# Kernel tuning notes

Measured on AMD Instinct MI355X. Metric: run time of the kernel, lower is better.

The kernel has to match this reference:

```python
import jax, jax.numpy as jnp
import numpy as np

B, C, H, W = 8, 64, 64, 64
R = 4
INTER = C // R   # 16
QK = C // 8      # 8
OUT = 64
EPS = 1e-5

def _bn(h, s, b, m, v):
    # inference-mode BatchNorm2d over channel dim of NCHW
    inv = s / jnp.sqrt(v + EPS)
    return h * inv[None, :, None, None] + (b - m * inv)[None, :, None, None]

def _conv1x1(h, w, b):
    # 1x1 conv == per-pixel matmul over channels
    return jnp.einsum('oc,bchw->bohw', w, h) + b[None, :, None, None]

def setup_inputs() -> dict:
    key = jax.random.key(0)
    ks = jax.random.split(key, 16)
    def wgt(k, shape):
        return jax.random.normal(k, shape, jnp.float32) * 0.05
    ones = lambda n: jnp.ones((n,), jnp.float32)
    zeros = lambda n: jnp.zeros((n,), jnp.float32)
    return {
        'x': jax.random.normal(ks[0], (B, C, H, W), jnp.float32),
        'lw1': wgt(ks[1], (INTER, C)), 'lb1': zeros(INTER),
        'ls1': ones(INTER), 'lbb1': zeros(INTER), 'lm1': zeros(INTER), 'lv1': ones(INTER),
        'lw2': wgt(ks[2], (C, INTER)), 'lb2': zeros(C),
        'ls2': ones(C), 'lbb2': zeros(C), 'lm2': zeros(C), 'lv2': ones(C),
        'gw1': wgt(ks[3], (INTER, C)), 'gb1': zeros(INTER),
        'gs1': ones(INTER), 'gbb1': zeros(INTER), 'gm1': zeros(INTER), 'gv1': ones(INTER),
        'gw2': wgt(ks[4], (C, INTER)), 'gb2': zeros(C),
        'gs2': ones(C), 'gbb2': zeros(C), 'gm2': zeros(C), 'gv2': ones(C),
        'qw': wgt(ks[5], (QK, C)), 'qb': zeros(QK),
        'kw': wgt(ks[6], (QK, C)), 'kb': zeros(QK),
        'vw': wgt(ks[7], (C, C)), 'vb': zeros(C),
        'gamma': jnp.zeros((1,), jnp.float32),  # torch init: zeros
        'cw': wgt(ks[8], (OUT, C, 3, 3)), 'cb': zeros(OUT),
        'cs': ones(OUT), 'cbb': zeros(OUT), 'cm': zeros(OUT), 'cv': ones(OUT),
    }

def reference(x, lw1, lb1, ls1, lbb1, lm1, lv1, lw2, lb2, ls2, lbb2, lm2, lv2,
              gw1, gb1, gs1, gbb1, gm1, gv1, gw2, gb2, gs2, gbb2, gm2, gv2,
              qw, qb, kw, kb, vw, vb, gamma, cw, cb, cs, cbb, cm, cv):
    # --- SE-style channel gating: local branch (per-pixel) + global branch (GAP) ---
    xl = _bn(_conv1x1(jax.nn.relu(_bn(_conv1x1(x, lw1, lb1), ls1, lbb1, lm1, lv1)), lw2, lb2),
             ls2, lbb2, lm2, lv2)
    g = x.mean(axis=(2, 3), keepdims=True)  # AdaptiveAvgPool2d(1) -> [B,C,1,1]
    xg = _bn(_conv1x1(jax.nn.relu(_bn(_conv1x1(g, gw1, gb1), gs1, gbb1, gm1, gv1)), gw2, gb2),
             gs2, gbb2, gm2, gv2)
    xo = x * jax.nn.sigmoid(xl + xg)
    # --- full spatial self-attention (bmm -> softmax -> bmm, unscaled) ---
    # NOTE: the original forward computes this, forms gamma*out + xo, then
    # immediately overwrites `out` with conv(xo); we reproduce that faithfully.
    b_, c_, h_, w_ = x.shape
    n = h_ * w_
    q = _conv1x1(x, qw, qb).reshape(b_, QK, n)
    k = _conv1x1(x, kw, kb).reshape(b_, QK, n)
    att = jax.nn.softmax(jnp.einsum('bcn,bcm->bnm', q, k), axis=-1)  # [B,N,N]
    v = _conv1x1(x, vw, vb).reshape(b_, c_, n)
    attn_out = jnp.einsum('bcm,bnm->bcn', v, att).reshape(b_, c_, h_, w_)
    _dead = gamma[0] * attn_out + xo  # discarded by original module
    # --- final 3x3 conv + BN + ReLU applied to the gated features xo ---
    y = jax.lax.conv_general_dilated(xo, cw, (1, 1), 'SAME',
                                     dimension_numbers=('NCHW', 'OIHW', 'NCHW'))
    y = y + cb[None, :, None, None]
    return jax.nn.relu(_bn(y, cs, cbb, cm, cv))
```

## Files before the change

kernel.cpp:

```cpp
#include <hip/hip_runtime.h>
#include <hip/hip_bf16.h>

#define NPIX 4096
#define FEPS 1e-5f

typedef __hip_bfloat16 bf16;
typedef __attribute__((ext_vector_type(8))) short bf16x8;
typedef __attribute__((ext_vector_type(4))) float f32x4;

#define OFF_FOLD 64
#define OFF_G    512
#define OFF_LW1  1024
#define OFF_LW2  2048
#define OFF_GW1  3072
#define OFF_GW2  4096
#define WSWZ_BYTES_OFF 20480
#define XO_BYTES_OFF   94208

template<typename T> __device__ __forceinline__ float ldf(const T* p);
template<> __device__ __forceinline__ float ldf<bf16>(const bf16* p)  { return __bfloat162float(*p); }
template<> __device__ __forceinline__ float ldf<float>(const float* p){ return *p; }

template<typename T> __device__ __forceinline__ void stf(T* p, float v);
template<> __device__ __forceinline__ void stf<bf16>(bf16* p, float v)  { *p = __float2bfloat16(v); }
template<> __device__ __forceinline__ void stf<float>(float* p, float v){ *p = v; }

__device__ __forceinline__ unsigned short f2bu(float f) {
    union { bf16 h; unsigned short u; } c; c.h = __float2bfloat16(f); return c.u;
}

__global__ void r4_probe(const unsigned* __restrict__ x, int* __restrict__ flag)
{
    int t = threadIdx.x;
    unsigned w = x[t];
    unsigned h = w & 0xffffu;
    int e = (int)((h >> 7) & 0xff);
    int hit = (h == 0u || (e >= 96 && e <= 160)) ? 1 : 0;
    unsigned long long m = __ballot(hit);
    if (t == 0) flag[0] = (__popcll(m) >= 40) ? 1 : 2;
}

struct PrepArgs4 { const void* p[30]; };

template<typename T, int ID>
__global__ void r4_prep(PrepArgs4 a, float* __restrict__ ws,
                        unsigned short* __restrict__ wswz)
{
    if (((const int*)ws)[0] != ID) return;
    const T* lw1  = (const T*)a.p[0];  const T* lb1  = (const T*)a.p[1];
    const T* ls1  = (const T*)a.p[2];  const T* lbb1 = (const T*)a.p[3];
    const T* lm1  = (const T*)a.p[4];  const T* lv1  = (const T*)a.p[5];
    const T* lw2  = (const T*)a.p[6];  const T* lb2  = (const T*)a.p[7];
    const T* ls2  = (const T*)a.p[8];  const T* lbb2 = (const T*)a.p[9];
    const T* lm2  = (const T*)a.p[10]; const T* lv2  = (const T*)a.p[11];
    const T* gw1  = (const T*)a.p[12]; const T* gb1  = (const T*)a.p[13];
    const T* gs1  = (const T*)a.p[14]; const T* gbb1 = (const T*)a.p[15];
    const T* gm1  = (const T*)a.p[16]; const T* gv1  = (const T*)a.p[17];
    const T* gw2  = (const T*)a.p[18]; const T* gb2  = (const T*)a.p[19];
    const T* gs2  = (const T*)a.p[20]; const T* gbb2 = (const T*)a.p[21];
    const T* gm2  = (const T*)a.p[22]; const T* gv2  = (const T*)a.p[23];
    const T* cw   = (const T*)a.p[24]; const T* cb   = (const T*)a.p[25];
    const T* cs   = (const T*)a.p[26]; const T* cbb  = (const T*)a.p[27];
    const T* cm   = (const T*)a.p[28]; const T* cv   = (const T*)a.p[29];

    int bx = blockIdx.x;
    int tid = threadIdx.x;
    if (bx < 16) {
        for (int e = tid; e < 2304; e += 256) {
            int E = bx * 2304 + e;
            int j = E & 7;
            int F = E >> 3;
            int l = F & 63;
            int g = (F >> 6) & 3;
            int ts = F >> 8;
            int s = ts & 1;
            int t = ts >> 1;
            int oc = g * 16 + (l & 15);
            int ic = s * 32 + (l >> 4) * 8 + j;
            wswz[E] = f2bu(ldf(cw + (oc * 64 + ic) * 9 + t));
        }
    } else if (bx == 16) {
        for (int e = tid; e < 4096; e += 256) {
            if (e < 1024)      ws[OFF_LW1 + e]        = ldf(lw1 + e);
            else if (e < 2048) ws[OFF_LW2 + e - 1024] = ldf(lw2 + e - 1024);
            else if (e < 3072) ws[OFF_GW1 + e - 2048] = ldf(gw1 + e - 2048);
            else               ws[OFF_GW2 + e - 3072] = ldf(gw2 + e - 3072);
        }
    } else {
        if (tid < 16) {
            float inv = ldf(ls1 + tid) * rsqrtf(ldf(lv1 + tid) + FEPS);
            ws[OFF_FOLD + 0  + tid] = inv;
            ws[OFF_FOLD + 16 + tid] = ldf(lb1 + tid) * inv + ldf(lbb1 + tid) - ldf(lm1 + tid) * inv;
            float ginv = ldf(gs1 + tid) * rsqrtf(ldf(gv1 + tid) + FEPS);
            ws[OFF_FOLD + 160 + tid] = ginv;
            ws[OFF_FOLD + 176 + tid] = ldf(gb1 + tid) * ginv + ldf(gbb1 + tid) - ldf(gm1 + tid) * ginv;
        }
        if (tid < 64) {
            float inv2 = ldf(ls2 + tid) * rsqrtf(ldf(lv2 + tid) + FEPS);
            ws[OFF_FOLD + 32 + tid] = inv2;
            ws[OFF_FOLD + 96 + tid] = ldf(lb2 + tid) * inv2 + ldf(lbb2 + tid) - ldf(lm2 + tid) * inv2;
            float ginv2 = ldf(gs2 + tid) * rsqrtf(ldf(gv2 + tid) + FEPS);
            ws[OFF_FOLD + 192 + tid] = ginv2;
            ws[OFF_FOLD + 256 + tid] = ldf(gb2 + tid) * ginv2 + ldf(gbb2 + tid) - ldf(gm2 + tid) * ginv2;
            float cinv = ldf(cs + tid) * rsqrtf(ldf(cv + tid) + FEPS);
            ws[OFF_FOLD + 320 + tid] = cinv;
            ws[OFF_FOLD + 384 + tid] = ldf(cb + tid) * cinv + ldf(cbb + tid) - ldf(cm + tid) * cinv;
        }
    }
}

template<typename T, int ID>
__global__ void r4_means(const void* __restrict__ xv, float* __restrict__ ws)
{
    if (((const int*)ws)[0] != ID) return;
    const T* x = (const T*)xv + (size_t)blockIdx.x * NPIX;
    int t = threadIdx.x;
    float s = 0.f;
#pragma unroll
    for (int i = 0; i < 16; ++i) s += ldf(x + t * 16 + i);
#pragma unroll
    for (int off = 32; off > 0; off >>= 1) s += __shfl_down(s, off, 64);
    __shared__ float red[4];
    if ((t & 63) == 0) red[t >> 6] = s;
    __syncthreads();
    if (t == 0)
        ws[OFF_G + blockIdx.x] = (red[0] + red[1] + red[2] + red[3]) * (1.0f / 4096.0f);
}

template<typename T, int ID>
__global__ void r4_gate(const void* __restrict__ xv, float* __restrict__ ws,
                        uint4* __restrict__ xo)
{
    if (((const int*)ws)[0] != ID) return;
    int b = blockIdx.x >> 5;
    int n = (blockIdx.x & 31) * 128 + threadIdx.x;
    int tid = threadIdx.x;

    __shared__ float t1[16];
    __shared__ float xg[64];
    if (tid < 16) {
        float s = 0.f;
#pragma unroll
        for (int c = 0; c < 64; ++c)
            s += ws[OFF_GW1 + tid * 64 + c] * ws[OFF_G + b * 64 + c];
        float z = ws[OFF_FOLD + 160 + tid] * s + ws[OFF_FOLD + 176 + tid];
        t1[tid] = fmaxf(z, 0.f);
    }
    __syncthreads();
    if (tid < 64) {
        float s = 0.f;
#pragma unroll
        for (int j = 0; j < 16; ++j)
            s += ws[OFF_GW2 + tid * 16 + j] * t1[j];
        xg[tid] = ws[OFF_FOLD + 192 + tid] * s + ws[OFF_FOLD + 256 + tid];
    }
    __syncthreads();

    const T* xb = (const T*)xv + (size_t)b * 64 * NPIX + n;
    float xr[64];
#pragma unroll
    for (int c = 0; c < 64; ++c) xr[c] = ldf(xb + c * NPIX);

    float h[16];
#pragma unroll
    for (int i = 0; i < 16; ++i) {
        float s = 0.f;
#pragma unroll
        for (int c = 0; c < 64; ++c) s += ws[OFF_LW1 + i * 64 + c] * xr[c];
        float z = ws[OFF_FOLD + 0 + i] * s + ws[OFF_FOLD + 16 + i];
        h[i] = fmaxf(z, 0.f);
    }

    uint4* xop = xo + ((size_t)b * NPIX + n) * 8;
#pragma unroll
    for (int cg = 0; cg < 8; ++cg) {
        unsigned v[8];
#pragma unroll
        for (int j = 0; j < 8; ++j) {
            int c = cg * 8 + j;
            float s = 0.f;
#pragma unroll
            for (int k = 0; k < 16; ++k) s += ws[OFF_LW2 + c * 16 + k] * h[k];
            float z = ws[OFF_FOLD + 32 + c] * s + ws[OFF_FOLD + 96 + c] + xg[c];
            float sg = 1.0f / (1.0f + __expf(-z));
            v[j] = (unsigned)f2bu(xr[c] * sg);
        }
        uint4 pk;
        pk.x = v[0] | (v[1] << 16);
        pk.y = v[2] | (v[3] << 16);
        pk.z = v[4] | (v[5] << 16);
        pk.w = v[6] | (v[7] << 16);
        xop[cg] = pk;
    }
}

template<typename T, int ID>
__global__ __launch_bounds__(128)
void r4_conv(const bf16x8* __restrict__ wsw, const float* __restrict__ ws,
             const char* __restrict__ xob_base, void* __restrict__ outv)
{
    if (((const int*)ws)[0] != ID) return;
    int bx  = blockIdx.x;
    int b   = bx >> 7;
    int r   = (bx >> 1) & 63;
    int c0  = (bx & 1) * 32;
    int tid = threadIdx.x;
    int w   = tid >> 6;
    int l   = tid & 63;
    int a   = l & 15;
    int q   = l >> 4;

    const char* xob = xob_base + (size_t)b * NPIX * 128;

    int  colOff[3][2];
    bool edge[3][2];
#pragma unroll
    for (int dci = 0; dci < 3; ++dci)
#pragma unroll
        for (int nf = 0; nf < 2; ++nf) {
            int c = c0 + nf * 16 + a + (dci - 1);
            edge[dci][nf] = (c < 0) || (c > 63);
            c = min(63, max(0, c));
            colOff[dci][nf] = c << 7;
        }

    const bf16x8 zf = {0, 0, 0, 0, 0, 0, 0, 0};
    f32x4 acc[2][2] = {};

#pragma unroll
    for (int t = 0; t < 9; ++t) {
        const int dr  = t / 3 - 1;
        const int dci = t % 3;
        int rr = r + dr;
        if (rr < 0 || rr > 63) continue;
        const char* rowp = xob + rr * 8192;
#pragma unroll
        for (int s = 0; s < 2; ++s) {
            bf16x8 A0 = wsw[((t * 2 + s) * 4 + 2 * w + 0) * 64 + l];
            bf16x8 A1 = wsw[((t * 2 + s) * 4 + 2 * w + 1) * 64 + l];
            int sq = s * 64 + q * 16;
#pragma unroll
            for (int nf = 0; nf < 2; ++nf) {
                bf16x8 B = *(const bf16x8*)(rowp + colOff[dci][nf] + sq);
                if (dci != 1) { if (edge[dci][nf]) B = zf; }
                acc[0][nf] = __builtin_amdgcn_mfma_f32_16x16x32_bf16(A0, B, acc[0][nf], 0, 0, 0);
                acc[1][nf] = __builtin_amdgcn_mfma_f32_16x16x32_bf16(A1, B, acc[1][nf], 0, 0, 0);
            }
        }
    }

    const float* cA = ws + OFF_FOLD + 320;
    const float* cB = ws + OFF_FOLD + 384;
    int pixBase = r * 64 + c0;
#pragma unroll
    for (int gi = 0; gi < 2; ++gi) {
        int g = 2 * w + gi;
#pragma unroll
        for (int reg = 0; reg < 4; ++reg) {
            int oc = g * 16 + q * 4 + reg;
            float Af = cA[oc];
            float Bf = cB[oc];
#pragma unroll
            for (int nf = 0; nf < 2; ++nf) {
                int pix = pixBase + nf * 16 + a;
                float y = fmaxf(acc[gi][nf][reg] * Af + Bf, 0.f);
                stf((T*)outv + ((size_t)b * 64 + oc) * NPIX + pix, y);
            }
        }
    }
}

extern "C" void kernel_launch(void* const* d_in, const int* in_sizes, int n_in,
                              void* d_out, int out_size, void* d_ws, size_t ws_size,
                              hipStream_t stream)
{
    (void)in_sizes; (void)n_in; (void)out_size; (void)ws_size;
    const void* x = d_in[0];
    float* ws = (float*)d_ws;
    unsigned short* wswz = (unsigned short*)((char*)d_ws + WSWZ_BYTES_OFF);
    char* xo = (char*)d_ws + XO_BYTES_OFF;

    PrepArgs4 pa;
    for (int i = 0; i < 24; ++i) pa.p[i] = d_in[1 + i];
    for (int i = 0; i < 6; ++i)  pa.p[24 + i] = d_in[32 + i];

    r4_probe<<<dim3(1), dim3(64), 0, stream>>>((const unsigned*)x, (int*)d_ws);

    r4_prep<bf16, 1><<<dim3(18), dim3(256), 0, stream>>>(pa, ws, wswz);
    r4_prep<float, 2><<<dim3(18), dim3(256), 0, stream>>>(pa, ws, wswz);

    r4_means<bf16, 1><<<dim3(512), dim3(256), 0, stream>>>(x, ws);
    r4_means<float, 2><<<dim3(512), dim3(256), 0, stream>>>(x, ws);

    r4_gate<bf16, 1><<<dim3(256), dim3(128), 0, stream>>>(x, ws, (uint4*)xo);
    r4_gate<float, 2><<<dim3(256), dim3(128), 0, stream>>>(x, ws, (uint4*)xo);

    r4_conv<bf16, 1><<<dim3(1024), dim3(128), 0, stream>>>(
        (const bf16x8*)wswz, ws, xo, d_out);
    r4_conv<float, 2><<<dim3(1024), dim3(128), 0, stream>>>(
        (const bf16x8*)wswz, ws, xo, d_out);
}
```

Baseline: 194.0 us.

## Merge dtype-specialized kernel pairs and vectorize bf16 loads in means and gate

Result: faster. 188.8 us (-2.6%).

```diff
diff --git a/kernel.cpp b/kernel.cpp
--- a/kernel.cpp
+++ b/kernel.cpp
@@ -28,8 +28,14 @@
 __device__ __forceinline__ unsigned short f2bu(float f) {
     union { bf16 h; unsigned short u; } c; c.h = __float2bfloat16(f); return c.u;
 }
-
-__global__ void r4_probe(const unsigned* __restrict__ x, int* __restrict__ flag)
+__device__ __forceinline__ float blo(unsigned u) {
+    union { unsigned i; float f; } c; c.i = u << 16; return c.f;
+}
+__device__ __forceinline__ float bhi(unsigned u) {
+    union { unsigned i; float f; } c; c.i = u & 0xffff0000u; return c.f;
+}
+
+__global__ void r5_probe(const unsigned* __restrict__ x, int* __restrict__ flag)
 {
     int t = threadIdx.x;
     unsigned w = x[t];
@@ -40,13 +46,12 @@
     if (t == 0) flag[0] = (__popcll(m) >= 40) ? 1 : 2;
 }
 
-struct PrepArgs4 { const void* p[30]; };
-
-template<typename T, int ID>
-__global__ void r4_prep(PrepArgs4 a, float* __restrict__ ws,
-                        unsigned short* __restrict__ wswz)
-{
-    if (((const int*)ws)[0] != ID) return;
+struct PrepArgs5 { const void* p[30]; };
+
+template<typename T>
+__device__ void prep_body(const PrepArgs5& a, float* __restrict__ ws,
+                          unsigned short* __restrict__ wswz)
+{
     const T* lw1  = (const T*)a.p[0];  const T* lb1  = (const T*)a.p[1];
     const T* ls1  = (const T*)a.p[2];  const T* lbb1 = (const T*)a.p[3];
     const T* lm1  = (const T*)a.p[4];  const T* lv1  = (const T*)a.p[5];
@@ -109,29 +114,47 @@
     }
 }
 
-template<typename T, int ID>
-__global__ void r4_means(const void* __restrict__ xv, float* __restrict__ ws)
-{
-    if (((const int*)ws)[0] != ID) return;
-    const T* x = (const T*)xv + (size_t)blockIdx.x * NPIX;
+__global__ void r5_prep(PrepArgs5 a, float* __restrict__ ws,
+                        unsigned short* __restrict__ wswz)
+{
+    if (((const int*)ws)[0] == 1) prep_body<bf16>(a, ws, wswz);
+    else                          prep_body<float>(a, ws, wswz);
+}
+
+__global__ void r5_means(const void* __restrict__ xv, float* __restrict__ ws)
+{
+    int flag = ((const int*)ws)[0];
+    int bc = blockIdx.x;
     int t = threadIdx.x;
     float s = 0.f;
-#pragma unroll
-    for (int i = 0; i < 16; ++i) s += ldf(x + t * 16 + i);
+    if (flag == 1) {
+        const uint4* p = (const uint4*)((const bf16*)xv + (size_t)bc * NPIX);
+#pragma unroll
+        for (int i = 0; i < 2; ++i) {
+            uint4 v = p[t * 2 + i];
+            s += blo(v.x) + bhi(v.x) + blo(v.y) + bhi(v.y)
+               + blo(v.z) + bhi(v.z) + blo(v.w) + bhi(v.w);
+        }
+    } else {
+        const float4* p = (const float4*)((const float*)xv + (size_t)bc * NPIX);
+#pragma unroll
+        for (int i = 0; i < 4; ++i) {
+            float4 v = p[t * 4 + i];
+            s += v.x + v.y + v.z + v.w;
+        }
+    }
 #pragma unroll
     for (int off = 32; off > 0; off >>= 1) s += __shfl_down(s, off, 64);
     __shared__ float red[4];
     if ((t & 63) == 0) red[t >> 6] = s;
     __syncthreads();
     if (t == 0)
-        ws[OFF_G + blockIdx.x] = (red[0] + red[1] + red[2] + red[3]) * (1.0f / 4096.0f);
-}
-
-template<typename T, int ID>
-__global__ void r4_gate(const void* __restrict__ xv, float* __restrict__ ws,
-                        uint4* __restrict__ xo)
-{
-    if (((const int*)ws)[0] != ID) return;
+        ws[OFF_G + bc] = (red[0] + red[1] + red[2] + red[3]) * (1.0f / 4096.0f);
+}
+
+__device__ void gate_slow_f32(const void* __restrict__ xv, float* __restrict__ ws,
+                              uint4* __restrict__ xo)
+{
     int b = blockIdx.x >> 5;
     int n = (blockIdx.x & 31) * 128 + threadIdx.x;
     int tid = threadIdx.x;
@@ -143,23 +166,21 @@
 #pragma unroll
         for (int c = 0; c < 64; ++c)
             s += ws[OFF_GW1 + tid * 64 + c] * ws[OFF_G + b * 64 + c];
-        float z = ws[OFF_FOLD + 160 + tid] * s + ws[OFF_FOLD + 176 + tid];
-        t1[tid] = fmaxf(z, 0.f);
+        t1[tid] = fmaxf(ws[OFF_FOLD + 160 + tid] * s + ws[OFF_FOLD + 176 + tid], 0.f);
     }
     __syncthreads();
     if (tid < 64) {
         float s = 0.f;
 #pragma unroll
-        for (int j = 0; j < 16; ++j)
-            s += ws[OFF_GW2 + tid * 16 + j] * t1[j];
+        for (int j = 0; j < 16; ++j) s += ws[OFF_GW2 + tid * 16 + j] * t1[j];
         xg[tid] = ws[OFF_FOLD + 192 + tid] * s + ws[OFF_FOLD + 256 + tid];
     }
     __syncthreads();
 
-    const T* xb = (const T*)xv + (size_t)b * 64 * NPIX + n;
+    const float* xb = (const float*)xv + (size_t)b * 64 * NPIX + n;
     float xr[64];
 #pragma unroll
-    for (int c = 0; c < 64; ++c) xr[c] = ldf(xb + c * NPIX);
+    for (int c = 0; c < 64; ++c) xr[c] = xb[c * NPIX];
 
     float h[16];
 #pragma unroll
@@ -167,8 +188,7 @@
         float s = 0.f;
 #pragma unroll
         for (int c = 0; c < 64; ++c) s += ws[OFF_LW1 + i * 64 + c] * xr[c];
-        float z = ws[OFF_FOLD + 0 + i] * s + ws[OFF_FOLD + 16 + i];
-        h[i] = fmaxf(z, 0.f);
+        h[i] = fmaxf(ws[OFF_FOLD + 0 + i] * s + ws[OFF_FOLD + 16 + i], 0.f);
     }
 
     uint4* xop = xo + ((size_t)b * NPIX + n) * 8;
@@ -182,8 +202,7 @@
 #pragma unroll
             for (int k = 0; k < 16; ++k) s += ws[OFF_LW2 + c * 16 + k] * h[k];
             float z = ws[OFF_FOLD + 32 + c] * s + ws[OFF_FOLD + 96 + c] + xg[c];
-            float sg = 1.0f / (1.0f + __expf(-z));
-            v[j] = (unsigned)f2bu(xr[c] * sg);
+            v[j] = (unsigned)f2bu(xr[c] / (1.0f + __expf(-z)));
         }
         uint4 pk;
         pk.x = v[0] | (v[1] << 16);
@@ -194,12 +213,90 @@
     }
 }
 
-template<typename T, int ID>
 __global__ __launch_bounds__(128)
-void r4_conv(const bf16x8* __restrict__ wsw, const float* __restrict__ ws,
-             const char* __restrict__ xob_base, void* __restrict__ outv)
-{
-    if (((const int*)ws)[0] != ID) return;
+void r5_gate(const void* __restrict__ xv, float* __restrict__ ws,
+             uint4* __restrict__ xo)
+{
+    if (((const int*)ws)[0] != 1) { gate_slow_f32(xv, ws, xo); return; }
+
+    int bx = blockIdx.x;
+    int b = bx >> 5;
+    int pix0 = (bx & 31) * 128;
+    int t = threadIdx.x;
+
+    __shared__ float t1[16];
+    __shared__ float xg[64];
+    __shared__ char tile[64 * 256];
+
+    const uint4* xsrc = (const uint4*)((const bf16*)xv + (size_t)b * 64 * NPIX + pix0);
+    uint4 ld[8];
+#pragma unroll
+    for (int k = 0; k < 8; ++k) {
+        int e = k * 128 + t;
+        int c = e >> 4;
+        int u = e & 15;
+        ld[k] = xsrc[(size_t)c * 512 + u];
+    }
+    if (t < 16) {
+        float s = 0.f;
+#pragma unroll
+        for (int c = 0; c < 64; ++c)
+            s += ws[OFF_GW1 + t * 64 + c] * ws[OFF_G + b * 64 + c];
+        t1[t] = fmaxf(ws[OFF_FOLD + 160 + t] * s + ws[OFF_FOLD + 176 + t], 0.f);
+    }
+#pragma unroll
+    for (int k = 0; k < 8; ++k) {
+        int e = k * 128 + t;
+        int c = e >> 4;
+        int u = e & 15;
+        *(uint4*)(tile + c * 256 + u * 16) = ld[k];
+    }
+    __syncthreads();
+    if (t < 64) {
+        float s = 0.f;
+#pragma unroll
+        for (int j = 0; j < 16; ++j) s += ws[OFF_GW2 + t * 16 + j] * t1[j];
+        xg[t] = ws[OFF_FOLD + 192 + t] * s + ws[OFF_FOLD + 256 + t];
+    }
+    float xr[64];
+#pragma unroll
+    for (int c = 0; c < 64; ++c)
+        xr[c] = __bfloat162float(*(const bf16*)(tile + c * 256 + t * 2));
+    float h[16];
+#pragma unroll
+    for (int i = 0; i < 16; ++i) {
+        float s = 0.f;
+#pragma unroll
+        for (int c = 0; c < 64; ++c) s += ws[OFF_LW1 + i * 64 + c] * xr[c];
+        h[i] = fmaxf(ws[OFF_FOLD + 0 + i] * s + ws[OFF_FOLD + 16 + i], 0.f);
+    }
+    __syncthreads();
+    uint4* xop = xo + ((size_t)b * NPIX + pix0 + t) * 8;
+#pragma unroll
+    for (int cg = 0; cg < 8; ++cg) {
+        unsigned v[8];
+#pragma unroll
+        for (int j = 0; j < 8; ++j) {
+            int c = cg * 8 + j;
+            float s = 0.f;
+#pragma unroll
+            for (int k = 0; k < 16; ++k) s += ws[OFF_LW2 + c * 16 + k] * h[k];
+            float z = ws[OFF_FOLD + 32 + c] * s + ws[OFF_FOLD + 96 + c] + xg[c];
+            v[j] = (unsigned)f2bu(xr[c] / (1.0f + __expf(-z)));
+        }
+        uint4 pk;
+        pk.x = v[0] | (v[1] << 16);
+        pk.y = v[2] | (v[3] << 16);
+        pk.z = v[4] | (v[5] << 16);
+        pk.w = v[6] | (v[7] << 16);
+        xop[cg] = pk;
+    }
+}
+
+template<typename T>
+__device__ void conv_body(const bf16x8* __restrict__ wsw, const float* __restrict__ ws,
+                          const char* __restrict__ xob_base, void* __restrict__ outv)
+{
     int bx  = blockIdx.x;
     int b   = bx >> 7;
     int r   = (bx >> 1) & 63;
@@ -270,6 +367,14 @@
     }
 }
 
+__global__ __launch_bounds__(128)
+void r5_conv(const bf16x8* __restrict__ wsw, const float* __restrict__ ws,
+             const char* __restrict__ xob_base, void* __restrict__ outv)
+{
+    if (((const int*)ws)[0] == 1) conv_body<bf16>(wsw, ws, xob_base, outv);
+    else                          conv_body<float>(wsw, ws, xob_base, outv);
+}
+
 extern "C" void kernel_launch(void* const* d_in, const int* in_sizes, int n_in,
                               void* d_out, int out_size, void* d_ws, size_t ws_size,
                               hipStream_t stream)
@@ -280,23 +385,14 @@
     unsigned short* wswz = (unsigned short*)((char*)d_ws + WSWZ_BYTES_OFF);
     char* xo = (char*)d_ws + XO_BYTES_OFF;
 
-    PrepArgs4 pa;
+    PrepArgs5 pa;
     for (int i = 0; i < 24; ++i) pa.p[i] = d_in[1 + i];
     for (int i = 0; i < 6; ++i)  pa.p[24 + i] = d_in[32 + i];
 
-    r4_probe<<<dim3(1), dim3(64), 0, stream>>>((const unsigned*)x, (int*)d_ws);
-
-    r4_prep<bf16, 1><<<dim3(18), dim3(256), 0, stream>>>(pa, ws, wswz);
-    r4_prep<float, 2><<<dim3(18), dim3(256), 0, stream>>>(pa, ws, wswz);
-
-    r4_means<bf16, 1><<<dim3(512), dim3(256), 0, stream>>>(x, ws);
-    r4_means<float, 2><<<dim3(512), dim3(256), 0, stream>>>(x, ws);
-
-    r4_gate<bf16, 1><<<dim3(256), dim3(128), 0, stream>>>(x, ws, (uint4*)xo);
-    r4_gate<float, 2><<<dim3(256), dim3(128), 0, stream>>>(x, ws, (uint4*)xo);
-
-    r4_conv<bf16, 1><<<dim3(1024), dim3(128), 0, stream>>>(
+    r5_probe<<<dim3(1), dim3(64), 0, stream>>>((const unsigned*)x, (int*)d_ws);
+    r5_prep<<<dim3(18), dim3(256), 0, stream>>>(pa, ws, wswz);
+    r5_means<<<dim3(512), dim3(256), 0, stream>>>(x, ws);
+    r5_gate<<<dim3(256), dim3(128), 0, stream>>>(x, ws, (uint4*)xo);
+    r5_conv<<<dim3(1024), dim3(128), 0, stream>>>(
         (const bf16x8*)wswz, ws, xo, d_out);
-    r4_conv<float, 2><<<dim3(1024), dim3(128), 0, stream>>>(
-        (const bf16x8*)wswz, ws, xo, d_out);
-}
+}
```
